# Performance work log

Measured on AMD Instinct MI355X. Metric: run time of the kernel, lower is better.

Reference implementation:

```python
import jax, jax.numpy as jnp
import numpy as np

N = 50000      # nodes
E = 800000     # edges (avg degree 16)
IN = 128
H = 128
OUT = 64
L = 3          # num GIN layers
G = 512        # graphs in batch
BN_EPS = 1e-5


def setup_inputs() -> dict:
    key = jax.random.key(0)
    ks = jax.random.split(key, 16)
    x = jax.random.normal(ks[0], (N, IN), dtype=jnp.float32)
    edge_index = jax.random.randint(ks[1], (2, E), 0, N, dtype=jnp.int64)
    batch = jnp.sort(jax.random.randint(ks[2], (N,), 0, G, dtype=jnp.int64))

    s_in = 1.0 / np.sqrt(IN)
    s_h = 1.0 / np.sqrt(H)
    # layer 0 has fan-in IN == H so we can stack all L layers uniformly
    conv_W1 = jax.random.normal(ks[3], (L, IN, H), dtype=jnp.float32) * s_in
    conv_b1 = jnp.zeros((L, H), dtype=jnp.float32)
    conv_gamma = jnp.ones((L, H), dtype=jnp.float32)
    conv_beta = jnp.zeros((L, H), dtype=jnp.float32)
    conv_W2 = jax.random.normal(ks[4], (L, H, H), dtype=jnp.float32) * s_h
    conv_b2 = jnp.zeros((L, H), dtype=jnp.float32)

    head_W1 = jax.random.normal(ks[5], (H, H), dtype=jnp.float32) * s_h
    head_b1 = jnp.zeros((H,), dtype=jnp.float32)
    head_W2 = jax.random.normal(ks[6], (H, OUT), dtype=jnp.float32) * s_h
    head_b2 = jnp.zeros((OUT,), dtype=jnp.float32)

    return dict(x=x, conv_W1=conv_W1, conv_b1=conv_b1, conv_gamma=conv_gamma,
                conv_beta=conv_beta, conv_W2=conv_W2, conv_b2=conv_b2,
                head_W1=head_W1, head_b1=head_b1, head_W2=head_W2,
                head_b2=head_b2, edge_index=edge_index, batch=batch)


def _mlp_bn(h, W1, b1, gamma, beta, W2, b2):
    # Linear -> BatchNorm (batch stats, biased var) -> ReLU -> Linear
    h = h @ W1 + b1
    mu = jnp.mean(h, axis=0)
    var = jnp.var(h, axis=0)
    h = (h - mu) * jax.lax.rsqrt(var + BN_EPS) * gamma + beta
    h = jax.nn.relu(h)
    return h @ W2 + b2


def reference(x, conv_W1, conv_b1, conv_gamma, conv_beta, conv_W2, conv_b2,
              head_W1, head_b1, head_W2, head_b2, edge_index, batch):
    src, dst = edge_index[0], edge_index[1]
    for l in range(L):
        # GINConv, eps=0: nn(x_i + sum_{j->i} x_j)
        agg = jax.ops.segment_sum(x[src], dst, num_segments=N)
        x = jax.nn.relu(_mlp_bn(x + agg, conv_W1[l], conv_b1[l],
                                conv_gamma[l], conv_beta[l],
                                conv_W2[l], conv_b2[l]))
    # global_add_pool -> [G, H]
    g = jax.ops.segment_sum(x, batch, num_segments=G)
    # head MLP (norm=None, dropout eval-mode identity)
    g = jax.nn.relu(g @ head_W1 + head_b1)
    return g @ head_W2 + head_b2
```

## Files before the change

### kernel.cpp

```cpp
#include <hip/hip_runtime.h>

#define N_NODES 50000
#define N_EDGES 800000
#define HDIM 128
#define ODIM 64
#define NLAYER 3
#define NGRAPH 512
#define BN_EPS 1e-5f
#define BCAP 48
#define NBUCKET 256
#define BRANGE 196
#define NBLK 782
#define GBLK 782
#define PROWS 64
#define HPITCH 136
#define TPITCH 136

#define SCAT_BLK 782
#define CVT_BLK 6250
#define CVTW_BLK 673

typedef __attribute__((ext_vector_type(8))) short short8;
typedef __attribute__((ext_vector_type(8))) unsigned short ushort8;
typedef __attribute__((ext_vector_type(4))) float floatx4;

static __device__ __forceinline__ unsigned short f2bf(float f) {
    union { float f; unsigned int u; } v; v.f = f;
    unsigned int r = v.u + 0x7FFFu + ((v.u >> 16) & 1u);
    return (unsigned short)(r >> 16);
}
static __device__ __forceinline__ float bf2f(unsigned short s) {
    union { unsigned int u; float f; } v; v.u = ((unsigned int)s) << 16;
    return v.f;
}


__global__ __launch_bounds__(256) void k_prep(
    const int* __restrict__ src, const int* __restrict__ dst,
    unsigned int* __restrict__ bstore,
    unsigned int* __restrict__ prefW,
    int* __restrict__ vcnt,
    const float* __restrict__ x, unsigned short* __restrict__ xa,
    const float* __restrict__ W1, const float* __restrict__ W2,
    const float* __restrict__ hW1, const float* __restrict__ hW2,
    unsigned short* __restrict__ wtb,
    float* __restrict__ p64all)
{
    int b = blockIdx.x;
    int tid = threadIdx.x;
    if (b < SCAT_BLK) {
        __shared__ int hist[NBUCKET], pos[NBUCKET];
        __shared__ int sa[NBUCKET], sb[NBUCKET];
        __shared__ unsigned int sed[1024];
        hist[tid] = 0;
        __syncthreads();

        int base = (b * 256 + tid) * 4;
        bool valid = base < N_EDGES;
        unsigned int ev[4]; int bk[4];
        if (valid) {
            int4 s4 = *(const int4*)(src + base);
            int4 d4 = *(const int4*)(dst + base);
            ev[0] = (unsigned)s4.x | ((unsigned)d4.x << 16); bk[0] = d4.x / BRANGE;
            ev[1] = (unsigned)s4.y | ((unsigned)d4.y << 16); bk[1] = d4.y / BRANGE;
            ev[2] = (unsigned)s4.z | ((unsigned)d4.z << 16); bk[2] = d4.z / BRANGE;
            ev[3] = (unsigned)s4.w | ((unsigned)d4.w << 16); bk[3] = d4.w / BRANGE;
            atomicAdd(&hist[bk[0]], 1); atomicAdd(&hist[bk[1]], 1);
            atomicAdd(&hist[bk[2]], 1); atomicAdd(&hist[bk[3]], 1);
        }
        __syncthreads();

        sa[tid] = hist[tid];
        __syncthreads();
        int* pin = sa; int* pout = sb;
#pragma unroll
        for (int d = 1; d < NBUCKET; d <<= 1) {
            pout[tid] = pin[tid] + ((tid >= d) ? pin[tid - d] : 0);
            __syncthreads();
            int* t = pin; pin = pout; pout = t;
        }
        int excl = (tid > 0) ? pin[tid - 1] : 0;
        pos[tid] = excl;
        prefW[(size_t)b * NBUCKET + tid] = (unsigned int)excl;
        if (tid == NBUCKET - 1) vcnt[b] = pin[NBUCKET - 1];
        __syncthreads();

        if (valid) {
#pragma unroll
            for (int j = 0; j < 4; ++j) {
                int p = atomicAdd(&pos[bk[j]], 1);
                sed[p] = ev[j];
            }
        }
        __syncthreads();

        unsigned int* out = bstore + (size_t)b * 1024;
#pragma unroll
        for (int j = 0; j < 4; ++j) out[tid * 4 + j] = sed[tid * 4 + j];
    } else if (b < SCAT_BLK + CVT_BLK) {
        int i = (b - SCAT_BLK) * 256 + tid;
        if (i < N_NODES * HDIM / 4) {
            float4 v = ((const float4*)x)[i];
            ushort4 o = make_ushort4(f2bf(v.x), f2bf(v.y), f2bf(v.z), f2bf(v.w));
            ((ushort4*)xa)[i] = o;
        }
    } else {
        int idx = (b - SCAT_BLK - CVT_BLK) * 256 + tid;
        if (idx < 6 * HDIM * HDIM) {
            int mat = idx >> 14;
            int rem = idx & 16383;
            int k = rem >> 7, n = rem & 127;
            int l = mat >> 1;
            const float* W = (mat & 1) ? (W2 + l * HDIM * HDIM) : (W1 + l * HDIM * HDIM);
            wtb[mat * HDIM * HDIM + n * HDIM + k] = f2bf(W[k * HDIM + n]);
        } else if (idx < 7 * HDIM * HDIM) {
            int j = idx - 6 * HDIM * HDIM;
            int n = j >> 7, k = j & 127;
            wtb[idx] = f2bf(hW1[k * HDIM + n]);
        } else if (idx < 7 * HDIM * HDIM + ODIM * HDIM) {
            int j = idx - 7 * HDIM * HDIM;
            int n = j >> 7, k = j & 127;
            wtb[idx] = f2bf(hW2[k * ODIM + n]);
        } else if (idx < 7 * HDIM * HDIM + ODIM * HDIM + HDIM) {
            xa[(size_t)N_NODES * HDIM + (idx - 7 * HDIM * HDIM - ODIM * HDIM)] = 0;
        } else if (idx < 7 * HDIM * HDIM + ODIM * HDIM + HDIM + NLAYER * PROWS * 256) {
            p64all[idx - (7 * HDIM * HDIM + ODIM * HDIM + HDIM)] = 0.f;
        }
    }
}


__global__ __launch_bounds__(256) void k_bucket(
    const unsigned int* __restrict__ bstore,
    const unsigned int* __restrict__ prefW,
    const int* __restrict__ vcnt,
    int* __restrict__ cnt,
    unsigned short* __restrict__ colidx)
{
    __shared__ __align__(16) unsigned short lb[BRANGE * BCAP];
    __shared__ int lc[BRANGE];
    int k = blockIdx.x;
    int tid = threadIdx.x;
    if (tid < BRANGE) lc[tid] = 0;
    __syncthreads();

    for (int b = tid; b < SCAT_BLK; b += 256) {
        int s = (int)prefW[(size_t)b * NBUCKET + k];
        int e = (k == NBUCKET - 1) ? vcnt[b] : (int)prefW[(size_t)b * NBUCKET + k + 1];
        const unsigned int* seg = bstore + (size_t)b * 1024;
        for (int i = s; i < e; ++i) {
            unsigned int ed = seg[i];
            int ld = (int)(ed >> 16) - k * BRANGE;
            int p = atomicAdd(&lc[ld], 1);
            if (p < BCAP) lb[ld * BCAP + p] = (unsigned short)(ed & 0xFFFFu);
        }
    }
    __syncthreads();

    for (int d = tid; d < BRANGE; d += 256) {
        int deg = lc[d]; if (deg > BCAP) deg = BCAP;
        int end = (deg + 7) & ~7;
        for (int i = deg; i < end; ++i) lb[d * BCAP + i] = (unsigned short)N_NODES;
        cnt[k * BRANGE + d] = deg;
    }
    __syncthreads();

    short8* dst8 = (short8*)(colidx + (size_t)k * BRANGE * BCAP);
    const short8* src8 = (const short8*)lb;
    for (int i = tid; i < (BRANGE * BCAP) / 8; i += 256) dst8[i] = src8[i];
}


__global__ __launch_bounds__(512, 6) void k_gml(
    const unsigned short* __restrict__ x,
    const int* __restrict__ cnt,
    const unsigned short* __restrict__ colidx,
    const unsigned short* __restrict__ wt,
    const float* __restrict__ b1,
    unsigned short* __restrict__ hout,
    float* __restrict__ p64)
{
    __shared__ float s_sum[HDIM], s_sq[HDIM];
    __shared__ __align__(16) unsigned short yb[64 * TPITCH];
    int tid = threadIdx.x;
    if (tid < HDIM) { s_sum[tid] = 0.f; s_sq[tid] = 0.f; }
    int nbase = blockIdx.x * 64;

#pragma unroll
    for (int t = tid; t < 1024; t += 512) {
        int nl = t >> 4;
        int seg = (t & 15) * 8;
        int gnode = nbase + nl;
        float acc[8] = {0.f, 0.f, 0.f, 0.f, 0.f, 0.f, 0.f, 0.f};
        if (gnode < N_NODES) {
            short8 v = *(const short8*)(x + (size_t)gnode * HDIM + seg);
#pragma unroll
            for (int j = 0; j < 8; ++j) acc[j] = bf2f((unsigned short)v[j]);
            int deg = cnt[gnode]; if (deg > BCAP) deg = BCAP;
            int e = gnode * BCAP;
            int end = e + ((deg + 7) & ~7);
            for (; e < end; e += 8) {
                ushort8 i0 = *(const ushort8*)(colidx + e);
                short8 v0 = *(const short8*)(x + (size_t)i0[0] * HDIM + seg);
                short8 v1 = *(const short8*)(x + (size_t)i0[1] * HDIM + seg);
                short8 v2 = *(const short8*)(x + (size_t)i0[2] * HDIM + seg);
                short8 v3 = *(const short8*)(x + (size_t)i0[3] * HDIM + seg);
                short8 v4 = *(const short8*)(x + (size_t)i0[4] * HDIM + seg);
                short8 v5 = *(const short8*)(x + (size_t)i0[5] * HDIM + seg);
                short8 v6 = *(const short8*)(x + (size_t)i0[6] * HDIM + seg);
                short8 v7 = *(const short8*)(x + (size_t)i0[7] * HDIM + seg);
#pragma unroll
                for (int j = 0; j < 8; ++j)
                    acc[j] += ((bf2f((unsigned short)v0[j]) + bf2f((unsigned short)v1[j])) +
                               (bf2f((unsigned short)v2[j]) + bf2f((unsigned short)v3[j]))) +
                              ((bf2f((unsigned short)v4[j]) + bf2f((unsigned short)v5[j])) +
                               (bf2f((unsigned short)v6[j]) + bf2f((unsigned short)v7[j])));
            }
        }
        short8 o;
#pragma unroll
        for (int j = 0; j < 8; ++j) o[j] = (short)f2bf(acc[j]);
        *(short8*)&yb[nl * TPITCH + seg] = o;
    }
    __syncthreads();

    int wv = tid >> 6, lane = tid & 63;
    int m = lane & 15, quad = lane >> 4;
    int mrow = (wv & 3) * 16 + m;
    int ncol0 = (wv >> 2) * 64;

    short8 a[4];
#pragma unroll
    for (int kk = 0; kk < 4; ++kk)
        a[kk] = *(const short8*)&yb[mrow * TPITCH + kk * 32 + quad * 8];
    __syncthreads();

    floatx4 acc4[4];
#pragma unroll
    for (int nt = 0; nt < 4; ++nt) {
        floatx4 c = {0.f, 0.f, 0.f, 0.f};
#pragma unroll
        for (int kk = 0; kk < 4; ++kk) {
            short8 b = *(const short8*)(wt + (ncol0 + nt * 16 + m) * HDIM + kk * 32 + quad * 8);
            c = __builtin_amdgcn_mfma_f32_16x16x32_bf16(a[kk], b, c, 0, 0, 0);
        }
        acc4[nt] = c;
    }

    int lrow0 = (wv & 3) * 16 + quad * 4;
#pragma unroll
    for (int nt = 0; nt < 4; ++nt) {
        int n = ncol0 + nt * 16 + m;
        float bias = b1[n];
        float ssum = 0.f, ssq = 0.f;
#pragma unroll
        for (int r = 0; r < 4; ++r) {
            float val = acc4[nt][r] + bias;
            yb[(lrow0 + r) * TPITCH + n] = f2bf(val);
            if (nbase + lrow0 + r < N_NODES) { ssum += val; ssq += val * val; }
        }
        atomicAdd(&s_sum[n], ssum);
        atomicAdd(&s_sq[n], ssq);
    }
    __syncthreads();
    if (tid < HDIM) {
        int prow = (blockIdx.x & (PROWS - 1)) * 256;
        atomicAdd(&p64[prow + tid], s_sum[tid]);
        atomicAdd(&p64[prow + HDIM + tid], s_sq[tid]);
    }
    int lrow = tid >> 3, off = (tid & 7) * 16;
    int grow = nbase + lrow;
    if (grow < N_NODES) {
        *(short8*)(hout + (size_t)grow * HDIM + off) = *(const short8*)&yb[lrow * TPITCH + off];
        *(short8*)(hout + (size_t)grow * HDIM + off + 8) = *(const short8*)&yb[lrow * TPITCH + off + 8];
    }
}


__global__ __launch_bounds__(256) void k_mlp2(
    const unsigned short* __restrict__ hin,
    const float* __restrict__ p64,
    const float* __restrict__ gamma,
    const float* __restrict__ beta,
    const unsigned short* __restrict__ wt,
    const float* __restrict__ b2,
    unsigned short* __restrict__ xout)
{
    __shared__ float red[256];
    __shared__ float s_scale[HDIM], s_shift[HDIM];
    __shared__ __align__(16) unsigned short tb[64 * TPITCH];
    int tid = threadIdx.x;

    {
        float s = 0.f;
#pragma unroll 8
        for (int i = 0; i < PROWS; ++i) s += p64[i * 256 + tid];
        red[tid] = s;
    }
    __syncthreads();
    if (tid < HDIM) {
        float mu = red[tid] * (1.f / N_NODES);
        float var = red[HDIM + tid] * (1.f / N_NODES) - mu * mu;
        float sc = gamma[tid] * rsqrtf(var + BN_EPS);
        s_scale[tid] = sc;
        s_shift[tid] = beta[tid] - mu * sc;
    }
    __syncthreads();

    int wv = tid >> 6, lane = tid & 63;
    int m = lane & 15, quad = lane >> 4;
    int row0 = blockIdx.x * 64 + wv * 16;
    int arow = row0 + m;

    short8 a[4];
    if (arow < N_NODES) {
#pragma unroll
        for (int kk = 0; kk < 4; ++kk) {
            short8 v = *(const short8*)(hin + (size_t)arow * HDIM + kk * 32 + quad * 8);
            int c0 = kk * 32 + quad * 8;
            short8 af;
#pragma unroll
            for (int j = 0; j < 8; ++j) {
                float f = fmaxf(bf2f((unsigned short)v[j]) * s_scale[c0 + j] + s_shift[c0 + j], 0.f);
                af[j] = (short)f2bf(f);
            }
            a[kk] = af;
        }
    } else {
#pragma unroll
        for (int kk = 0; kk < 4; ++kk) a[kk] = (short8)0;
    }

    floatx4 acc[8];
#pragma unroll
    for (int nt = 0; nt < 8; ++nt) {
        floatx4 c = {0.f, 0.f, 0.f, 0.f};
#pragma unroll
        for (int kk = 0; kk < 4; ++kk) {
            short8 b = *(const short8*)(wt + (nt * 16 + m) * HDIM + kk * 32 + quad * 8);
            c = __builtin_amdgcn_mfma_f32_16x16x32_bf16(a[kk], b, c, 0, 0, 0);
        }
        acc[nt] = c;
    }

    int lrow0 = wv * 16 + quad * 4;
#pragma unroll
    for (int nt = 0; nt < 8; ++nt) {
        int n = nt * 16 + m;
        float bias = b2[n];
#pragma unroll
        for (int r = 0; r < 4; ++r)
            tb[(lrow0 + r) * TPITCH + n] = f2bf(fmaxf(acc[nt][r] + bias, 0.f));
    }
    __syncthreads();
    int lrow = tid >> 2, off = (tid & 3) * 32;
    int grow = blockIdx.x * 64 + lrow;
    if (grow < N_NODES) {
#pragma unroll
        for (int i = 0; i < 4; ++i)
            *(short8*)(xout + (size_t)grow * HDIM + off + i * 8) =
                *(const short8*)&tb[lrow * TPITCH + off + i * 8];
    }
}


__global__ __launch_bounds__(256) void k_pool(
    const unsigned short* __restrict__ xf,
    const int* __restrict__ batch,
    unsigned short* __restrict__ g)
{
    __shared__ float red[16][HDIM];
    int gid = blockIdx.x;
    int tid = threadIdx.x;

    int lo = 0, hi = N_NODES;
    while (lo < hi) { int mid = (lo + hi) >> 1; if (batch[mid] < gid) lo = mid + 1; else hi = mid; }
    int start = lo;
    int lo2 = start, hi2 = N_NODES;
    while (lo2 < hi2) { int mid = (lo2 + hi2) >> 1; if (batch[mid] < gid + 1) lo2 = mid + 1; else hi2 = mid; }
    int end = lo2;

    int tsub = tid & 15, rgrp = tid >> 4;
    int seg = tsub * 8;
    float acc[8] = {0.f, 0.f, 0.f, 0.f, 0.f, 0.f, 0.f, 0.f};
    for (int r = start + rgrp; r < end; r += 16) {
        short8 v = *(const short8*)(xf + (size_t)r * HDIM + seg);
#pragma unroll
        for (int j = 0; j < 8; ++j) acc[j] += bf2f((unsigned short)v[j]);
    }
#pragma unroll
    for (int j = 0; j < 8; ++j) red[rgrp][seg + j] = acc[j];
    __syncthreads();
    if (tid < HDIM) {
        float s = 0.f;
#pragma unroll
        for (int i = 0; i < 16; ++i) s += red[i][tid];
        g[gid * HDIM + tid] = f2bf(s);
    }
}


__global__ __launch_bounds__(256) void k_head(
    const unsigned short* __restrict__ g,
    const unsigned short* __restrict__ w1t,
    const float* __restrict__ b1,
    const unsigned short* __restrict__ w2t,
    const float* __restrict__ b2,
    float* __restrict__ out)
{
    __shared__ unsigned short tb[64 * HPITCH];
    int tid = threadIdx.x;
    int wv = tid >> 6, lane = tid & 63;
    int m = lane & 15, quad = lane >> 4;
    int row0 = blockIdx.x * 64 + wv * 16;

    short8 a[4];
#pragma unroll
    for (int kk = 0; kk < 4; ++kk)
        a[kk] = *(const short8*)(g + (size_t)(row0 + m) * HDIM + kk * 32 + quad * 8);

#pragma unroll
    for (int nt = 0; nt < 8; ++nt) {
        floatx4 c = {0.f, 0.f, 0.f, 0.f};
#pragma unroll
        for (int kk = 0; kk < 4; ++kk) {
            short8 b = *(const short8*)(w1t + (nt * 16 + m) * HDIM + kk * 32 + quad * 8);
            c = __builtin_amdgcn_mfma_f32_16x16x32_bf16(a[kk], b, c, 0, 0, 0);
        }
        int n = nt * 16 + m;
        float bias = b1[n];
#pragma unroll
        for (int r = 0; r < 4; ++r) {
            int lrow = wv * 16 + quad * 4 + r;
            tb[lrow * HPITCH + n] = f2bf(fmaxf(c[r] + bias, 0.f));
        }
    }
    __syncthreads();

    short8 a2[4];
#pragma unroll
    for (int kk = 0; kk < 4; ++kk)
        a2[kk] = *(const short8*)&tb[(wv * 16 + m) * HPITCH + kk * 32 + quad * 8];

#pragma unroll
    for (int nt = 0; nt < 4; ++nt) {
        floatx4 c = {0.f, 0.f, 0.f, 0.f};
#pragma unroll
        for (int kk = 0; kk < 4; ++kk) {
            short8 b = *(const short8*)(w2t + (nt * 16 + m) * HDIM + kk * 32 + quad * 8);
            c = __builtin_amdgcn_mfma_f32_16x16x32_bf16(a2[kk], b, c, 0, 0, 0);
        }
        int n = nt * 16 + m;
        float bias = b2[n];
#pragma unroll
        for (int r = 0; r < 4; ++r) {
            int row = row0 + quad * 4 + r;
            out[(size_t)row * ODIM + n] = c[r] + bias;
        }
    }
}


extern "C" void kernel_launch(void* const* d_in, const int* in_sizes, int n_in,
                              void* d_out, int out_size, void* d_ws, size_t ws_size,
                              hipStream_t stream) {
    const float* x        = (const float*)d_in[0];
    const float* conv_W1  = (const float*)d_in[1];
    const float* conv_b1  = (const float*)d_in[2];
    const float* conv_g   = (const float*)d_in[3];
    const float* conv_be  = (const float*)d_in[4];
    const float* conv_W2  = (const float*)d_in[5];
    const float* conv_b2  = (const float*)d_in[6];
    const float* head_W1  = (const float*)d_in[7];
    const float* head_b1  = (const float*)d_in[8];
    const float* head_W2  = (const float*)d_in[9];
    const float* head_b2  = (const float*)d_in[10];
    const int*   edges    = (const int*)d_in[11];
    const int*   batch    = (const int*)d_in[12];

    char* ws = (char*)d_ws;
    int*            cnt    = (int*)(ws + 0);
    unsigned short* colidx = (unsigned short*)(ws + 200704);
    unsigned short* wtb    = (unsigned short*)(ws + 5017600);
    float*          part64 = (float*)(ws + 5263360);
    unsigned int*   bstore = (unsigned int*)(ws + 5459968);
    unsigned int*   prefW  = (unsigned int*)(ws + 8663040);
    int*            vcnt   = (int*)(ws + 9463808);
    unsigned short* gbuf   = (unsigned short*)(ws + 9467008);
    unsigned short* xa     = (unsigned short*)(ws + 9598080);
    unsigned short* xb     = (unsigned short*)(ws + 22398336);
    (void)in_sizes; (void)n_in; (void)out_size; (void)ws_size;


    k_prep<<<SCAT_BLK + CVT_BLK + CVTW_BLK, 256, 0, stream>>>(
        edges, edges + N_EDGES, bstore, prefW, vcnt, x, xa,
        conv_W1, conv_W2, head_W1, head_W2, wtb, part64);
    k_bucket<<<NBUCKET, 256, 0, stream>>>(bstore, prefW, vcnt, cnt, colidx);

    for (int l = 0; l < NLAYER; ++l) {
        k_gml<<<GBLK, 512, 0, stream>>>(xa, cnt, colidx,
                                        wtb + (2 * l) * HDIM * HDIM,
                                        conv_b1 + l * HDIM, xb,
                                        part64 + (size_t)l * PROWS * 256);
        k_mlp2<<<NBLK, 256, 0, stream>>>(xb, part64 + (size_t)l * PROWS * 256,
                                         conv_g + l * HDIM, conv_be + l * HDIM,
                                         wtb + (2 * l + 1) * HDIM * HDIM,
                                         conv_b2 + l * HDIM, xa);
    }

    k_pool<<<NGRAPH, 256, 0, stream>>>(xa, batch, gbuf);
    k_head<<<NGRAPH / 64, 256, 0, stream>>>(gbuf, wtb + 6 * HDIM * HDIM, head_b1,
                                            wtb + 7 * HDIM * HDIM, head_b2,
                                            (float*)d_out);
}
```

Before: 387.3 us.

## Store node features as FP8 e4m3 for neighbor gathers

Node features read by the aggregation gather are now quantized to FP8 e4m3 bytes instead of bf16. The goal is to halve gather traffic. Dequantization goes through a 256-entry shared-memory lookup table built in each block. The last layer still writes bf16 for pooling. FP8 loses a lot of precision on activations (values below 2^-6 flush to zero) and risks tolerance failures, and the LDS table lookups add bank-conflict cost. The diff also leaves a stray no-op LDS read.

```diff
diff --git a/kernel.cpp b/kernel.cpp
--- a/kernel.cpp
+++ b/kernel.cpp
@@ -22,6 +22,8 @@
 
 typedef __attribute__((ext_vector_type(8))) short short8;
 typedef __attribute__((ext_vector_type(8))) unsigned short ushort8;
+typedef __attribute__((ext_vector_type(8))) unsigned char uchar8x;
+typedef __attribute__((ext_vector_type(4))) unsigned char uchar4x;
 typedef __attribute__((ext_vector_type(4))) float floatx4;
 
 static __device__ __forceinline__ unsigned short f2bf(float f) {
@@ -32,6 +34,20 @@
 static __device__ __forceinline__ float bf2f(unsigned short s) {
     union { unsigned int u; float f; } v; v.u = ((unsigned int)s) << 16;
     return v.f;
+}
+static __device__ __forceinline__ unsigned char f2e4(float f) {
+    union { float f; unsigned int u; } v; v.f = f;
+    unsigned char s = (unsigned char)((v.u >> 24) & 0x80u);
+    float a = fabsf(f);
+    if (a >= 448.f) return (unsigned char)(s | 0x7Eu);
+    if (a < 0.015625f) return s;
+    v.f = a;
+    unsigned int r = v.u + 0x7FFFFu + ((v.u >> 20) & 1u);
+    int e8 = (int)((r >> 23) & 0xFF) - 127 + 7;
+    unsigned int man = (r >> 20) & 0x7u;
+    if (e8 <= 0) return s;
+    if (e8 > 15) return (unsigned char)(s | 0x7Eu);
+    return (unsigned char)(s | ((unsigned)e8 << 3) | man);
 }
 
 
@@ -40,7 +56,7 @@
     unsigned int* __restrict__ bstore,
     unsigned int* __restrict__ prefW,
     int* __restrict__ vcnt,
-    const float* __restrict__ x, unsigned short* __restrict__ xa,
+    const float* __restrict__ x, unsigned char* __restrict__ xa,
     const float* __restrict__ W1, const float* __restrict__ W2,
     const float* __restrict__ hW1, const float* __restrict__ hW2,
     unsigned short* __restrict__ wtb,
@@ -101,8 +117,9 @@
         int i = (b - SCAT_BLK) * 256 + tid;
         if (i < N_NODES * HDIM / 4) {
             float4 v = ((const float4*)x)[i];
-            ushort4 o = make_ushort4(f2bf(v.x), f2bf(v.y), f2bf(v.z), f2bf(v.w));
-            ((ushort4*)xa)[i] = o;
+            uchar4x o;
+            o[0] = f2e4(v.x); o[1] = f2e4(v.y); o[2] = f2e4(v.z); o[3] = f2e4(v.w);
+            ((uchar4x*)xa)[i] = o;
         }
     } else {
         int idx = (b - SCAT_BLK - CVT_BLK) * 256 + tid;
@@ -172,7 +189,7 @@
 
 
 __global__ __launch_bounds__(512, 6) void k_gml(
-    const unsigned short* __restrict__ x,
+    const unsigned char* __restrict__ x,
     const int* __restrict__ cnt,
     const unsigned short* __restrict__ colidx,
     const unsigned short* __restrict__ wt,
@@ -181,9 +198,18 @@
     float* __restrict__ p64)
 {
     __shared__ float s_sum[HDIM], s_sq[HDIM];
+    __shared__ float lut[256];
     __shared__ __align__(16) unsigned short yb[64 * TPITCH];
     int tid = threadIdx.x;
     if (tid < HDIM) { s_sum[tid] = 0.f; s_sq[tid] = 0.f; }
+    if (tid < 256) {
+        unsigned em = tid & 0x7F;
+        float mag;
+        if (em >= 8) { union { unsigned u; float f; } v; v.u = (em + 960u) << 20; mag = v.f; }
+        else mag = (float)em * 0.001953125f;
+        lut[tid] = (tid & 0x80) ? -mag : mag;
+    }
+    __syncthreads();
     int nbase = blockIdx.x * 64;
 
 #pragma unroll
@@ -193,33 +219,32 @@
         int gnode = nbase + nl;
         float acc[8] = {0.f, 0.f, 0.f, 0.f, 0.f, 0.f, 0.f, 0.f};
         if (gnode < N_NODES) {
-            short8 v = *(const short8*)(x + (size_t)gnode * HDIM + seg);
-#pragma unroll
-            for (int j = 0; j < 8; ++j) acc[j] = bf2f((unsigned short)v[j]);
+            uchar8x v = *(const uchar8x*)(x + (size_t)gnode * HDIM + seg);
+#pragma unroll
+            for (int j = 0; j < 8; ++j) acc[j] = lut[v[j]];
             int deg = cnt[gnode]; if (deg > BCAP) deg = BCAP;
             int e = gnode * BCAP;
             int end = e + ((deg + 7) & ~7);
             for (; e < end; e += 8) {
                 ushort8 i0 = *(const ushort8*)(colidx + e);
-                short8 v0 = *(const short8*)(x + (size_t)i0[0] * HDIM + seg);
-                short8 v1 = *(const short8*)(x + (size_t)i0[1] * HDIM + seg);
-                short8 v2 = *(const short8*)(x + (size_t)i0[2] * HDIM + seg);
-                short8 v3 = *(const short8*)(x + (size_t)i0[3] * HDIM + seg);
-                short8 v4 = *(const short8*)(x + (size_t)i0[4] * HDIM + seg);
-                short8 v5 = *(const short8*)(x + (size_t)i0[5] * HDIM + seg);
-                short8 v6 = *(const short8*)(x + (size_t)i0[6] * HDIM + seg);
-                short8 v7 = *(const short8*)(x + (size_t)i0[7] * HDIM + seg);
+                uchar8x v0 = *(const uchar8x*)(x + (size_t)i0[0] * HDIM + seg);
+                uchar8x v1 = *(const uchar8x*)(x + (size_t)i0[1] * HDIM + seg);
+                uchar8x v2 = *(const uchar8x*)(x + (size_t)i0[2] * HDIM + seg);
+                uchar8x v3 = *(const uchar8x*)(x + (size_t)i0[3] * HDIM + seg);
+                uchar8x v4 = *(const uchar8x*)(x + (size_t)i0[4] * HDIM + seg);
+                uchar8x v5 = *(const uchar8x*)(x + (size_t)i0[5] * HDIM + seg);
+                uchar8x v6 = *(const uchar8x*)(x + (size_t)i0[6] * HDIM + seg);
+                uchar8x v7 = *(const uchar8x*)(x + (size_t)i0[7] * HDIM + seg);
 #pragma unroll
                 for (int j = 0; j < 8; ++j)
-                    acc[j] += ((bf2f((unsigned short)v0[j]) + bf2f((unsigned short)v1[j])) +
-                               (bf2f((unsigned short)v2[j]) + bf2f((unsigned short)v3[j]))) +
-                              ((bf2f((unsigned short)v4[j]) + bf2f((unsigned short)v5[j])) +
-                               (bf2f((unsigned short)v6[j]) + bf2f((unsigned short)v7[j])));
+                    acc[j] += ((lut[v0[j]] + lut[v1[j]]) + (lut[v2[j]] + lut[v3[j]])) +
+                              ((lut[v4[j]] + lut[v5[j]]) + (lut[v6[j]] + lut[v7[j]]));
             }
         }
         short8 o;
 #pragma unroll
         for (int j = 0; j < 8; ++j) o[j] = (short)f2bf(acc[j]);
+        *(short8*)&yb[nl * TPITCH + seg * 2];
         *(short8*)&yb[nl * TPITCH + seg] = o;
     }
     __syncthreads();
@@ -284,7 +309,9 @@
     const float* __restrict__ beta,
     const unsigned short* __restrict__ wt,
     const float* __restrict__ b2,
-    unsigned short* __restrict__ xout)
+    unsigned char* __restrict__ xq,
+    unsigned short* __restrict__ xbf,
+    int last)
 {
     __shared__ float red[256];
     __shared__ float s_scale[HDIM], s_shift[HDIM];
@@ -353,13 +380,24 @@
             tb[(lrow0 + r) * TPITCH + n] = f2bf(fmaxf(acc[nt][r] + bias, 0.f));
     }
     __syncthreads();
-    int lrow = tid >> 2, off = (tid & 3) * 32;
+    int lrow = tid >> 2, offd = (tid & 3) * 32;
     int grow = blockIdx.x * 64 + lrow;
     if (grow < N_NODES) {
-#pragma unroll
-        for (int i = 0; i < 4; ++i)
-            *(short8*)(xout + (size_t)grow * HDIM + off + i * 8) =
-                *(const short8*)&tb[lrow * TPITCH + off + i * 8];
+        if (last) {
+#pragma unroll
+            for (int i = 0; i < 4; ++i)
+                *(short8*)(xbf + (size_t)grow * HDIM + offd + i * 8) =
+                    *(const short8*)&tb[lrow * TPITCH + offd + i * 8];
+        } else {
+#pragma unroll
+            for (int i = 0; i < 4; ++i) {
+                short8 vv = *(const short8*)&tb[lrow * TPITCH + offd + i * 8];
+                uchar8x q;
+#pragma unroll
+                for (int j = 0; j < 8; ++j) q[j] = f2e4(bf2f((unsigned short)vv[j]));
+                *(uchar8x*)(xq + (size_t)grow * HDIM + offd + i * 8) = q;
+            }
+        }
     }
 }
 
@@ -487,8 +525,8 @@
     unsigned int*   prefW  = (unsigned int*)(ws + 8663040);
     int*            vcnt   = (int*)(ws + 9463808);
     unsigned short* gbuf   = (unsigned short*)(ws + 9467008);
-    unsigned short* xa     = (unsigned short*)(ws + 9598080);
-    unsigned short* xb     = (unsigned short*)(ws + 22398336);
+    unsigned char*  xa     = (unsigned char*)(ws + 9598080);
+    unsigned short* xb     = (unsigned short*)(ws + 15998208);
     (void)in_sizes; (void)n_in; (void)out_size; (void)ws_size;
 
 
@@ -505,10 +543,11 @@
         k_mlp2<<<NBLK, 256, 0, stream>>>(xb, part64 + (size_t)l * PROWS * 256,
                                          conv_g + l * HDIM, conv_be + l * HDIM,
                                          wtb + (2 * l + 1) * HDIM * HDIM,
-                                         conv_b2 + l * HDIM, xa);
-    }
-
-    k_pool<<<NGRAPH, 256, 0, stream>>>(xa, batch, gbuf);
+                                         conv_b2 + l * HDIM, xa, xb,
+                                         (l == NLAYER - 1) ? 1 : 0);
+    }
+
+    k_pool<<<NGRAPH, 256, 0, stream>>>(xb, batch, gbuf);
     k_head<<<NGRAPH / 64, 256, 0, stream>>>(gbuf, wtb + 6 * HDIM * HDIM, head_b1,
                                             wtb + 7 * HDIM * HDIM, head_b2,
                                             (float*)d_out);
```

Measured after the change: 404.3 us. 4.4% more time.
